# Kernel optimization log

Hardware: AMD Instinct MI355X
Metric: run time of the kernel (lower is better)

## Reference

```python
import jax, jax.numpy as jnp
import numpy as np

# BigBird-roberta-base config with block_size=64, 12 layers
B = 1; S = 2048; D = 768; F = 3072; V = 50358
L = 12; H = 12; HD = 64; BS = 64; NB = S // BS; R = 3
NEG = -1.0e9
NKB = 5 + R           # global(2) + window(3) + random(3) key blocks per query block
NK = NKB * BS         # gathered keys per query block


def _block_map(nb, r, seed=0):
    """Static per-query-block key-block indices + dedup mask (first occurrence kept)."""
    rng = np.random.default_rng(seed)
    idx = np.zeros((nb, 5 + r), np.int32)
    dedup = np.ones((nb, 5 + r), np.float32)
    for i in range(nb):
        lst = [0, nb - 1, max(i - 1, 0), i, min(i + 1, nb - 1)]
        cand = np.setdiff1d(np.arange(nb), np.array(lst))
        lst += list(rng.choice(cand, r, replace=False))
        seen = set()
        for j, b in enumerate(lst):
            idx[i, j] = int(b)
            if b in seen:
                dedup[i, j] = 0.0
            seen.add(int(b))
    return idx, dedup

BLK_IDX, BLK_DEDUP = _block_map(NB, R)


def layer_norm(x, s, b):
    m = jnp.mean(x, axis=-1, keepdims=True)
    v = jnp.mean(jnp.square(x - m), axis=-1, keepdims=True)
    return (x - m) * jax.lax.rsqrt(v + 1e-12) * s + b


def bigbird_attn(x, wq, wk, wv, bq, bk, bv, wo, bo, key_mask):
    # x: [B,S,D]; key_mask: [B,S] float (1=keep)
    q = (x @ wq + bq).reshape(B, S, H, HD).transpose(0, 2, 1, 3)  # [B,H,S,HD]
    k = (x @ wk + bk).reshape(B, S, H, HD).transpose(0, 2, 1, 3)
    v = (x @ wv + bv).reshape(B, S, H, HD).transpose(0, 2, 1, 3)
    scale = 1.0 / np.sqrt(HD)
    qb = q.reshape(B, H, NB, BS, HD)
    kb = k.reshape(B, H, NB, BS, HD)
    vb = v.reshape(B, H, NB, BS, HD)
    # gather sparse key/value blocks: [B,H,NB,NKB,BS,HD] -> [B,H,NB,NK,HD]
    kg = kb[:, :, BLK_IDX].reshape(B, H, NB, NK, HD)
    vg = vb[:, :, BLK_IDX].reshape(B, H, NB, NK, HD)
    scores = jnp.einsum('bhnqd,bhnkd->bhnqk', qb, kg) * scale  # [B,H,NB,BS,NK]
    kmb = key_mask.reshape(B, NB, BS)[:, BLK_IDX]               # [B,NB,NKB,BS]
    m = (kmb * BLK_DEDUP[None, :, :, None]).reshape(B, 1, NB, 1, NK)
    probs = jax.nn.softmax(scores + (1.0 - m) * NEG, axis=-1)
    ctx = jnp.einsum('bhnqk,bhnkd->bhnqd', probs, vg)           # [B,H,NB,BS,HD]
    # global query blocks (first & last) attend densely to all keys
    qg = jnp.concatenate([qb[:, :, 0], qb[:, :, -1]], axis=2)   # [B,H,2*BS,HD]
    sg = jnp.einsum('bhqd,bhkd->bhqk', qg, k) * scale
    sg = sg + (1.0 - key_mask[:, None, None, :]) * NEG
    cg = jnp.einsum('bhqk,bhkd->bhqd', jax.nn.softmax(sg, axis=-1), v)
    ctx = ctx.at[:, :, 0].set(cg[:, :, :BS]).at[:, :, -1].set(cg[:, :, BS:])
    ctx = ctx.reshape(B, H, S, HD).transpose(0, 2, 1, 3).reshape(B, S, D)
    return ctx @ wo + bo


def setup_inputs() -> dict:
    key = jax.random.key(0)
    ks = jax.random.split(key, 16)
    p = lambda k, shape: jax.random.normal(k, shape, jnp.float32) * 0.02
    return {
        'input_ids': jax.random.randint(ks[0], (B, S), 0, V),
        'attention_mask': jnp.ones((B, S), jnp.int32),
        'token_type_ids': jnp.zeros((B, S), jnp.int32),
        'word_emb': p(ks[1], (V, D)),
        'pos_emb': p(ks[2], (S, D)),
        'type_emb': p(ks[3], (2, D)),
        'emb_ln_s': jnp.ones((D,)), 'emb_ln_b': jnp.zeros((D,)),
        'Wq': p(ks[4], (L, D, D)), 'Wk': p(ks[5], (L, D, D)), 'Wv': p(ks[6], (L, D, D)),
        'bq': jnp.zeros((L, D)), 'bk': jnp.zeros((L, D)), 'bv': jnp.zeros((L, D)),
        'Wo': p(ks[7], (L, D, D)), 'bo': jnp.zeros((L, D)),
        'ln1_s': jnp.ones((L, D)), 'ln1_b': jnp.zeros((L, D)),
        'W1': p(ks[8], (L, D, F)), 'b1': jnp.zeros((L, F)),
        'W2': p(ks[9], (L, F, D)), 'b2': jnp.zeros((L, D)),
        'ln2_s': jnp.ones((L, D)), 'ln2_b': jnp.zeros((L, D)),
        'fc_w': p(ks[10], (D, V)), 'fc_b': jnp.zeros((V,)),
    }


def reference(input_ids, attention_mask, token_type_ids, word_emb, pos_emb, type_emb,
              emb_ln_s, emb_ln_b, Wq, Wk, Wv, bq, bk, bv, Wo, bo, ln1_s, ln1_b,
              W1, b1, W2, b2, ln2_s, ln2_b, fc_w, fc_b):
    x = word_emb[input_ids] + pos_emb[None] + type_emb[token_type_ids]
    x = layer_norm(x, emb_ln_s, emb_ln_b)
    km = attention_mask.astype(x.dtype)
    for l in range(L):
        a = bigbird_attn(x, Wq[l], Wk[l], Wv[l], bq[l], bk[l], bv[l], Wo[l], bo[l], km)
        x = layer_norm(x + a, ln1_s[l], ln1_b[l])
        hdd = jax.nn.gelu(x @ W1[l] + b1[l])
        x = layer_norm(x + hdd @ W2[l] + b2[l], ln2_s[l], ln2_b[l])
    return x @ fc_w + fc_b  # logits [B,S,V]
```

## Files before the change

### kernel.cpp

```cpp
#include <hip/hip_runtime.h>
#include <hip/hip_bf16.h>


#define S_LEN 2048
#define DMODEL 768
#define FFDIM 3072
#define VOCAB 50358
#define VPAD  50432
#define NLAYER 12
#define NHEAD 12
#define NB 32
#define NKB 8
#define QKVN 2304

typedef __attribute__((ext_vector_type(8))) short bfrag8;
typedef __attribute__((ext_vector_type(8))) unsigned short us8;
typedef __attribute__((ext_vector_type(4))) float facc4;

__device__ __forceinline__ unsigned short f2bf(float f) {
  unsigned int u = __builtin_bit_cast(unsigned int, f);
  u += 0x7fffu + ((u >> 16) & 1u);
  return (unsigned short)(u >> 16);
}
__device__ __forceinline__ float bf2f(unsigned short h) {
  unsigned int u = ((unsigned int)h) << 16;
  return __builtin_bit_cast(float, u);
}

#define MFMA16(a, b, c) __builtin_amdgcn_mfma_f32_16x16x32_bf16((a), (b), (c), 0, 0, 0)
#define GLDS16(g, l) __builtin_amdgcn_global_load_lds( \
    (const __attribute__((address_space(1))) void*)(g), \
    (__attribute__((address_space(3))) void*)(l), 16, 0, 0)

struct Pcg {
  unsigned long long hi, lo, inc_hi, inc_lo;
  int has32; unsigned int buf32;
};

__device__ __forceinline__ void pcg_step(Pcg& p) {
  const unsigned long long MH = 0x2360ed051fc65da4ull;
  const unsigned long long ML = 0x4385df649fccf645ull;
  unsigned long long rl = p.lo * ML;
  unsigned long long rh = __umul64hi(p.lo, ML) + p.lo * MH + p.hi * ML;
  unsigned long long nl = rl + p.inc_lo;
  unsigned long long nh = rh + p.inc_hi + (nl < rl ? 1ull : 0ull);
  p.lo = nl; p.hi = nh;
}
__device__ __forceinline__ unsigned long long pcg_next64(Pcg& p) {
  pcg_step(p);
  unsigned int rot = (unsigned int)(p.hi >> 58);
  unsigned long long x = p.hi ^ p.lo;
  return (x >> rot) | (x << ((64u - rot) & 63u));
}
__device__ __forceinline__ unsigned int pcg_next32(Pcg& p) {
  if (p.has32) { p.has32 = 0; return p.buf32; }
  unsigned long long n = pcg_next64(p);
  p.has32 = 1; p.buf32 = (unsigned int)(n >> 32);
  return (unsigned int)n;
}
__device__ __forceinline__ unsigned int lemire32(Pcg& p, unsigned int rng) {
  unsigned int rng_excl = rng + 1u;
  unsigned long long m = (unsigned long long)pcg_next32(p) * (unsigned long long)rng_excl;
  unsigned int leftover = (unsigned int)m;
  if (leftover < rng_excl) {
    unsigned int threshold = (0xffffffffu - rng) % rng_excl;
    while (leftover < threshold) {
      m = (unsigned long long)pcg_next32(p) * (unsigned long long)rng_excl;
      leftover = (unsigned int)m;
    }
  }
  return (unsigned int)(m >> 32);
}

__global__ void blockmap_kernel(int* __restrict__ blk_idx, float* __restrict__ dedup) {
  if (threadIdx.x != 0 || blockIdx.x != 0) return;
  unsigned int pool[4];
  unsigned int hc = 0x43b0d7e5u;
  auto ss_hash = [&hc](unsigned int val) {
    val ^= hc; hc *= 0x931e8875u; val *= hc; val ^= val >> 16; return val;
  };
  auto ss_mix = [](unsigned int x, unsigned int y) {
    unsigned int r = 0xca01f9ddu * x - 0x4973f715u * y;
    r ^= r >> 16; return r;
  };
  for (int i = 0; i < 4; ++i) pool[i] = ss_hash(0u);
  for (int s = 0; s < 4; ++s)
    for (int d = 0; d < 4; ++d)
      if (s != d) pool[d] = ss_mix(pool[d], ss_hash(pool[s]));
  unsigned int st32[8];
  unsigned int hb = 0x8b51f9ddu;
  for (int i = 0; i < 8; ++i) {
    unsigned int dv = pool[i & 3];
    dv ^= hb; hb *= 0x58f38dedu; dv *= hb; dv ^= dv >> 16;
    st32[i] = dv;
  }
  unsigned long long sd[4];
  for (int i = 0; i < 4; ++i)
    sd[i] = (unsigned long long)st32[2*i] | ((unsigned long long)st32[2*i+1] << 32);
  Pcg p;
  p.inc_hi = (sd[2] << 1) | (sd[3] >> 63);
  p.inc_lo = (sd[3] << 1) | 1ull;
  p.hi = 0ull; p.lo = 0ull;
  pcg_step(p);
  unsigned long long ol = p.lo;
  p.lo = ol + sd[1];
  p.hi = p.hi + sd[0] + (p.lo < ol ? 1ull : 0ull);
  pcg_step(p);
  p.has32 = 0; p.buf32 = 0;

  for (int i = 0; i < NB; ++i) {
    int lst[8];
    lst[0] = 0; lst[1] = NB - 1;
    lst[2] = (i > 0) ? i - 1 : 0;
    lst[3] = i;
    lst[4] = (i + 1 < NB - 1) ? i + 1 : NB - 1;
    bool excl[NB];
    for (int c = 0; c < NB; ++c) excl[c] = false;
    for (int j = 0; j < 5; ++j) excl[lst[j]] = true;
    int cand[NB], n = 0;
    for (int c = 0; c < NB; ++c) if (!excl[c]) cand[n++] = c;
    long long idx[3];
    unsigned long long hs[4] = {~0ull, ~0ull, ~0ull, ~0ull};
    for (int tI = 0; tI < 3; ++tI) {
      unsigned long long j = (unsigned long long)(n - 3 + tI);
      unsigned long long val = (unsigned long long)lemire32(p, (unsigned int)j);
      unsigned long long loc = val & 3ull;
      while (hs[loc] != ~0ull && hs[loc] != val) loc = (loc + 1ull) & 3ull;
      if (hs[loc] == ~0ull) { hs[loc] = val; idx[tI] = (long long)val; }
      else {
        loc = j & 3ull;
        while (hs[loc] != ~0ull) loc = (loc + 1ull) & 3ull;
        hs[loc] = j; idx[tI] = (long long)j;
      }
    }
    for (int fi = 2; fi >= 1; --fi) {
      int fj = (int)lemire32(p, (unsigned int)fi);
      long long tmpv = idx[fi]; idx[fi] = idx[fj]; idx[fj] = tmpv;
    }
    lst[5] = cand[idx[0]]; lst[6] = cand[idx[1]]; lst[7] = cand[idx[2]];

    unsigned int seen = 0u;
    for (int j = 0; j < 8; ++j) {
      blk_idx[i*8 + j] = lst[j];
      dedup[i*8 + j] = ((seen >> lst[j]) & 1u) ? 0.0f : 1.0f;
      seen |= (1u << lst[j]);
    }
  }
}

__global__ __launch_bounds__(256) void tconv_kernel(
    const float* __restrict__ src, unsigned short* __restrict__ dst,
    int K, int N, size_t src_stride, size_t dst_stride) {
  __shared__ float tile[64][65];
  src += (size_t)blockIdx.z * src_stride;
  dst += (size_t)blockIdx.z * dst_stride;
  int n0 = blockIdx.x * 64, k0 = blockIdx.y * 64;
  int t = threadIdx.x;
  int tr = t >> 4, tc = (t & 15) * 4;
  if ((N & 3) == 0 && n0 + 64 <= N) {
    #pragma unroll
    for (int i = 0; i < 4; ++i) {
      int k = k0 + tr + i * 16;
      float4 v = *reinterpret_cast<const float4*>(src + (size_t)k * N + n0 + tc);
      tile[tr + i*16][tc + 0] = v.x; tile[tr + i*16][tc + 1] = v.y;
      tile[tr + i*16][tc + 2] = v.z; tile[tr + i*16][tc + 3] = v.w;
    }
  } else if ((N & 1) == 0 && n0 + 64 <= N) {
    #pragma unroll
    for (int i = 0; i < 4; ++i) {
      int k = k0 + tr + i * 16;
      float2 v0 = *reinterpret_cast<const float2*>(src + (size_t)k * N + n0 + tc);
      float2 v1 = *reinterpret_cast<const float2*>(src + (size_t)k * N + n0 + tc + 2);
      tile[tr + i*16][tc + 0] = v0.x; tile[tr + i*16][tc + 1] = v0.y;
      tile[tr + i*16][tc + 2] = v1.x; tile[tr + i*16][tc + 3] = v1.y;
    }
  } else {
    for (int i = 0; i < 4; ++i) {
      int k = k0 + tr + i * 16;
      #pragma unroll
      for (int q2 = 0; q2 < 4; ++q2) {
        int n = n0 + tc + q2;
        tile[tr + i*16][tc + q2] = (n < N) ? src[(size_t)k * N + n] : 0.0f;
      }
    }
  }
  __syncthreads();
  int wr_ = t >> 2, wc_ = (t & 3) * 16;
  us8 w0, w1;
  #pragma unroll
  for (int j = 0; j < 8; ++j) {
    w0[j] = f2bf(tile[wc_ + j][wr_]);
    w1[j] = f2bf(tile[wc_ + 8 + j][wr_]);
  }
  size_t b = (size_t)(n0 + wr_) * K + k0 + wc_;
  *reinterpret_cast<us8*>(dst + b) = w0;
  *reinterpret_cast<us8*>(dst + b + 8) = w1;
}

__global__ void bias_cat_kernel(const float* __restrict__ bq, const float* __restrict__ bk,
                                const float* __restrict__ bv, float* __restrict__ dst) {
  int l = blockIdx.x;
  for (int i = threadIdx.x; i < QKVN; i += blockDim.x) {
    float v = (i < 768) ? bq[l*768 + i] : (i < 1536) ? bk[l*768 + i - 768] : bv[l*768 + i - 1536];
    dst[l*QKVN + i] = v;
  }
}

__device__ __forceinline__ float block_sum256(float v, float* red) {
  for (int off = 32; off > 0; off >>= 1) v += __shfl_down(v, off);
  int wv = threadIdx.x >> 6;
  if ((threadIdx.x & 63) == 0) red[wv] = v;
  __syncthreads();
  float r = red[0] + red[1] + red[2] + red[3];
  __syncthreads();
  return r;
}

__global__ void embed_ln_kernel(const int* __restrict__ ids, const int* __restrict__ tts,
                                const float* __restrict__ we, const float* __restrict__ pe,
                                const float* __restrict__ te, const float* __restrict__ lns,
                                const float* __restrict__ lnb, float* __restrict__ x,
                                unsigned short* __restrict__ xh) {
  __shared__ float red[4];
  int row = blockIdx.x, t = threadIdx.x;
  int id = ids[row], ty = tts[row];
  float e[3]; float s = 0.0f;
  for (int j = 0; j < 3; ++j) {
    int d = t + 256*j;
    e[j] = we[(size_t)id*DMODEL + d] + pe[(size_t)row*DMODEL + d] + te[(size_t)ty*DMODEL + d];
    s += e[j];
  }
  float mean = block_sum256(s, red) * (1.0f/768.0f);
  float vs = 0.0f;
  for (int j = 0; j < 3; ++j) { float dd = e[j] - mean; vs += dd*dd; }
  float var = block_sum256(vs, red) * (1.0f/768.0f);
  float inv = rsqrtf(var + 1e-12f);
  for (int j = 0; j < 3; ++j) {
    int d = t + 256*j;
    float val = (e[j] - mean) * inv * lns[d] + lnb[d];
    size_t idx = (size_t)row*DMODEL + d;
    x[idx] = val;
    xh[idx] = f2bf(val);
  }
}

__global__ void resln_kernel(float* __restrict__ x, const float* __restrict__ a,
                             const float* __restrict__ lns, const float* __restrict__ lnb,
                             unsigned short* __restrict__ xh) {
  __shared__ float red[4];
  int row = blockIdx.x, t = threadIdx.x;
  float e[3]; float s = 0.0f;
  for (int j = 0; j < 3; ++j) {
    int d = t + 256*j;
    e[j] = x[(size_t)row*DMODEL + d] + a[(size_t)row*DMODEL + d];
    s += e[j];
  }
  float mean = block_sum256(s, red) * (1.0f/768.0f);
  float vs = 0.0f;
  for (int j = 0; j < 3; ++j) { float dd = e[j] - mean; vs += dd*dd; }
  float var = block_sum256(vs, red) * (1.0f/768.0f);
  float inv = rsqrtf(var + 1e-12f);
  for (int j = 0; j < 3; ++j) {
    int d = t + 256*j;
    float val = (e[j] - mean) * inv * lns[d] + lnb[d];
    size_t idx = (size_t)row*DMODEL + d;
    x[idx] = val;
    xh[idx] = f2bf(val);
  }
}

template<int BM, int NBUF, int TN, int OMODE, int ACT>
__global__ __launch_bounds__(256) void gemm13_kernel(
    const unsigned short* __restrict__ A_g, const unsigned short* __restrict__ Bt,
    const float* __restrict__ bias,
    float* __restrict__ Cf, unsigned short* __restrict__ Ch,
    int K, int Nreal) {
  __shared__ alignas(16) unsigned short As[NBUF][BM][32];
  __shared__ alignas(16) unsigned short Bs[NBUF][TN][32];
  constexpr int MFR = BM / 32;
  constexpr int NFR = (TN == 128) ? 4 : 2;
  constexpr int ACALLS = BM / 64;
  constexpr int NLOADS = ACALLS + ((TN == 128) ? 2 : 1);
  constexpr int DEPTH = NBUF - 2;
  int t = threadIdx.x;
  int mb = (int)gridDim.x;
  int nwg = mb * (int)gridDim.y;
  int lin = (int)blockIdx.x + mb * (int)blockIdx.y;
  int cpx = nwg >> 3;
  int nl = (lin & 7) * cpx + (lin >> 3);
  int m0 = (nl % mb) * BM, n0 = (nl / mb) * TN;

  int wave = t >> 6, lane = t & 63, l16 = lane & 15, lk = lane >> 4;
  int wr = wave >> 1, wc = wave & 1;
  int row16 = lane >> 2, seg4 = lane & 3;
  const int srcoff = (seg4 ^ ((row16 >> 1) & 3)) * 8;
  const int swzrd = (lk ^ ((l16 >> 1) & 3)) * 8;

  const unsigned short* ag = A_g + (size_t)(m0 + wave*(BM/4) + row16) * K + srcoff;
  const unsigned short* bg = Bt + (size_t)(n0 + (TN == 128 ? wave*32 : wave*16) + row16) * K + srcoff;
  const size_t K16 = (size_t)16 * K;

  auto STAGE = [&](int buf, int kit) {
    int k0 = kit << 5;
    #pragma unroll
    for (int j = 0; j < ACALLS; ++j)
      GLDS16(ag + (size_t)j * K16 + k0, &As[buf][wave*(BM/4) + 16*j][0]);
    if constexpr (TN == 128) {
      GLDS16(bg + k0, &Bs[buf][wave*32][0]);
      GLDS16(bg + K16 + k0, &Bs[buf][wave*32 + 16][0]);
    } else {
      GLDS16(bg + k0, &Bs[buf][wave*16][0]);
    }
  };

  facc4 acc[MFR][NFR];
  #pragma unroll
  for (int mi = 0; mi < MFR; ++mi)
    #pragma unroll
    for (int ni = 0; ni < NFR; ++ni)
      acc[mi][ni] = (facc4){0.f, 0.f, 0.f, 0.f};

  const int nk = K >> 5;
  STAGE(0, 0);
  if constexpr (DEPTH == 2) STAGE(1, 1);
  int cur = 0;
  for (int it = 0; it < nk; ++it) {
    if constexpr (DEPTH == 2) {
      if (it + 2 < nk) {
        STAGE((cur + 2) % NBUF, it + 2);
        asm volatile("s_waitcnt vmcnt(%0)" :: "n"(2 * NLOADS) : "memory");
      } else if (it + 1 < nk) {
        asm volatile("s_waitcnt vmcnt(%0)" :: "n"(NLOADS) : "memory");
      } else {
        asm volatile("s_waitcnt vmcnt(0)" ::: "memory");
      }
    } else {
      if (it + 1 < nk) {
        STAGE((cur + 1) % NBUF, it + 1);
        asm volatile("s_waitcnt vmcnt(%0)" :: "n"(NLOADS) : "memory");
      } else {
        asm volatile("s_waitcnt vmcnt(0)" ::: "memory");
      }
    }
    __builtin_amdgcn_sched_barrier(0);
    __builtin_amdgcn_s_barrier();
    __builtin_amdgcn_sched_barrier(0);
    bfrag8 af[MFR], bf[NFR];
    #pragma unroll
    for (int mi = 0; mi < MFR; ++mi)
      af[mi] = *reinterpret_cast<const bfrag8*>(&As[cur][wr*(BM/2) + mi*16 + l16][swzrd]);
    #pragma unroll
    for (int ni = 0; ni < NFR; ++ni)
      bf[ni] = *reinterpret_cast<const bfrag8*>(&Bs[cur][(TN == 128 ? wc*64 : wc*32) + ni*16 + l16][swzrd]);
    #pragma unroll
    for (int mi = 0; mi < MFR; ++mi)
      #pragma unroll
      for (int ni = 0; ni < NFR; ++ni)
        acc[mi][ni] = MFMA16(af[mi], bf[ni], acc[mi][ni]);
    cur = (cur + 1) % NBUF;
  }

  #pragma unroll
  for (int mi = 0; mi < MFR; ++mi)
    #pragma unroll
    for (int ni = 0; ni < NFR; ++ni) {
      int col = n0 + (TN == 128 ? wc*64 : wc*32) + ni*16 + l16;
      if (col >= Nreal) continue;
      float bv = bias[col];
      #pragma unroll
      for (int r2 = 0; r2 < 4; ++r2) {
        int row = m0 + wr*(BM/2) + mi*16 + lk*4 + r2;
        float val = acc[mi][ni][r2] + bv;
        if (ACT == 1) {
          float xx = val;
          val = 0.5f * xx * (1.0f + tanhf(0.7978845608028654f * (xx + 0.044715f * xx * xx * xx)));
        }
        size_t idx = (size_t)row * Nreal + col;
        if (OMODE == 0) Cf[idx] = val;
        else Ch[idx] = f2bf(val);
      }
    }
}

__device__ __forceinline__ void stage_glds64_swz(unsigned short (*dst)[64],
    const unsigned short* __restrict__ src, int ld, int t) {
  int w = t >> 6, lane = t & 63;
  int row8 = lane >> 3;
  int seg = (lane & 7) ^ (row8 & 7);
  const unsigned short* s = src + (size_t)(w*16 + row8) * ld + seg * 8;
  GLDS16(s, &dst[w*16][0]);
  GLDS16(s + (size_t)8 * ld, &dst[w*16 + 8][0]);
}

__global__ __launch_bounds__(256) void attn_kernel(
    const unsigned short* __restrict__ qkvh,
    const int* __restrict__ blk_idx, const float* __restrict__ dedup,
    const int* __restrict__ amask,
    unsigned short* __restrict__ ctxh,
    float* __restrict__ go, float* __restrict__ gm, float* __restrict__ gl) {
  __shared__ alignas(16) unsigned short Qs[64][64];
  __shared__ alignas(16) unsigned short KV2[2][64][64];
  __shared__ alignas(16) unsigned short Vs[64][66];
  __shared__ alignas(16) unsigned short Pt[64][68];
  int h = blockIdx.y;
  int bx = (int)blockIdx.x;
  const bool is_glob = (bx >= 30);
  int g = is_glob ? ((bx - 30) >> 2) : 0;
  int part = is_glob ? ((bx - 30) & 3) : 0;
  int qi = is_glob ? (g ? (NB - 1) : 0) : (bx + 1);
  int t = threadIdx.x, wave = t >> 6, lane = t & 63, l16 = lane & 15, lk = lane >> 4;
  const int swq0 = ((lk ^ (l16 & 7))) * 8;
  const int swq1 = (((4 + lk) ^ (l16 & 7))) * 8;
  const int vrow = t >> 2, vcolb = (t & 3) * 16;

  int barr[8];
  float addm[8][4];
  #pragma unroll
  for (int kb = 0; kb < 8; ++kb)
    barr[kb] = is_glob ? (part*8 + kb) : blk_idx[qi*NKB + kb];
  #pragma unroll
  for (int kb = 0; kb < 8; ++kb) {
    float dd = is_glob ? 1.0f : dedup[qi*NKB + kb];
    #pragma unroll
    for (int ni = 0; ni < 4; ++ni) {
      float mk = (float)amask[barr[kb]*64 + ni*16 + l16] * dd;
      addm[kb][ni] = (1.0f - mk) * (-1.0e9f);
    }
  }

  stage_glds64_swz(Qs, qkvh + (size_t)(qi*64)*QKVN + h*64, QKVN, t);
  __syncthreads();
  const bfrag8 q0 = *reinterpret_cast<const bfrag8*>(&Qs[wave*16 + l16][swq0]);
  const bfrag8 q1 = *reinterpret_cast<const bfrag8*>(&Qs[wave*16 + l16][swq1]);

  float mrow[4] = {-3.0e38f, -3.0e38f, -3.0e38f, -3.0e38f};
  float lrow[4] = {0.f, 0.f, 0.f, 0.f};
  facc4 o[4];
  #pragma unroll
  for (int ni = 0; ni < 4; ++ni) o[ni] = (facc4){0.f, 0.f, 0.f, 0.f};

  stage_glds64_swz(KV2[0], qkvh + (size_t)(barr[0]*64)*QKVN + DMODEL + h*64, QKVN, t);
  __builtin_amdgcn_sched_barrier(0);
  us8 vA0, vA1, vB0, vB1;
  {
    const unsigned short* vs0 = qkvh + (size_t)(barr[0]*64 + vrow)*QKVN + 2*DMODEL + h*64 + vcolb;
    vA0 = *reinterpret_cast<const us8*>(vs0);
    vA1 = *reinterpret_cast<const us8*>(vs0 + 8);
  }

  auto body = [&](int kb, const us8& vc0, const us8& vc1, us8& vn0, us8& vn1) {
    if (kb + 1 < 8) {
      int bn = barr[kb + 1];
      stage_glds64_swz(KV2[(kb + 1) & 1], qkvh + (size_t)(bn*64)*QKVN + DMODEL + h*64, QKVN, t);
      __builtin_amdgcn_sched_barrier(0);
      const unsigned short* vsn = qkvh + (size_t)(bn*64 + vrow)*QKVN + 2*DMODEL + h*64 + vcolb;
      vn0 = *reinterpret_cast<const us8*>(vsn);
      vn1 = *reinterpret_cast<const us8*>(vsn + 8);
      asm volatile("s_waitcnt vmcnt(4)" ::: "memory");
    } else {
      asm volatile("s_waitcnt vmcnt(0)" ::: "memory");
    }
    __builtin_amdgcn_sched_barrier(0);
    __builtin_amdgcn_s_barrier();
    __builtin_amdgcn_sched_barrier(0);
    float s[4][4];
    #pragma unroll
    for (int ni = 0; ni < 4; ++ni) {
      bfrag8 k0 = *reinterpret_cast<const bfrag8*>(&KV2[kb & 1][ni*16 + l16][swq0]);
      bfrag8 k1 = *reinterpret_cast<const bfrag8*>(&KV2[kb & 1][ni*16 + l16][swq1]);
      facc4 sa = (facc4){0.f, 0.f, 0.f, 0.f};
      sa = MFMA16(q0, k0, sa);
      sa = MFMA16(q1, k1, sa);
      #pragma unroll
      for (int r = 0; r < 4; ++r) s[ni][r] = sa[r] * 0.125f + addm[kb][ni];
    }
    float pexp[4][4];
    #pragma unroll
    for (int r = 0; r < 4; ++r) {
      float tm = fmaxf(fmaxf(s[0][r], s[1][r]), fmaxf(s[2][r], s[3][r]));
      tm = fmaxf(tm, __shfl_xor(tm, 1));
      tm = fmaxf(tm, __shfl_xor(tm, 2));
      tm = fmaxf(tm, __shfl_xor(tm, 4));
      tm = fmaxf(tm, __shfl_xor(tm, 8));
      float mn = fmaxf(mrow[r], tm);
      float f = expf(mrow[r] - mn);
      #pragma unroll
      for (int ni = 0; ni < 4; ++ni) o[ni][r] *= f;
      float ps = 0.0f;
      #pragma unroll
      for (int ni = 0; ni < 4; ++ni) { pexp[ni][r] = expf(s[ni][r] - mn); ps += pexp[ni][r]; }
      ps += __shfl_xor(ps, 1);
      ps += __shfl_xor(ps, 2);
      ps += __shfl_xor(ps, 4);
      ps += __shfl_xor(ps, 8);
      lrow[r] = lrow[r] * f + ps;
      mrow[r] = mn;
    }
    #pragma unroll
    for (int ni = 0; ni < 4; ++ni)
      #pragma unroll
      for (int r = 0; r < 4; ++r)
        Pt[wave*16 + lk*4 + r][ni*16 + l16] = f2bf(pexp[ni][r]);
    #pragma unroll
    for (int j = 0; j < 8; ++j) {
      Vs[vcolb + j][vrow] = vc0[j];
      Vs[vcolb + 8 + j][vrow] = vc1[j];
    }
    asm volatile("s_waitcnt lgkmcnt(0)" ::: "memory");
    __builtin_amdgcn_sched_barrier(0);
    __builtin_amdgcn_s_barrier();
    __builtin_amdgcn_sched_barrier(0);
    #pragma unroll
    for (int kc = 0; kc < 2; ++kc) {
      bfrag8 ph = *reinterpret_cast<const bfrag8*>(&Pt[wave*16 + l16][kc*32 + lk*8]);
      #pragma unroll
      for (int ni = 0; ni < 4; ++ni) {
        bfrag8 vh = *reinterpret_cast<const bfrag8*>(&Vs[ni*16 + l16][kc*32 + lk*8]);
        o[ni] = MFMA16(ph, vh, o[ni]);
      }
    }
  };

  body(0, vA0, vA1, vB0, vB1);
  body(1, vB0, vB1, vA0, vA1);
  body(2, vA0, vA1, vB0, vB1);
  body(3, vB0, vB1, vA0, vA1);
  body(4, vA0, vA1, vB0, vB1);
  body(5, vB0, vB1, vA0, vA1);
  body(6, vA0, vA1, vB0, vB1);
  body(7, vB0, vB1, vA0, vA1);

  if (!is_glob) {
    float invl[4];
    #pragma unroll
    for (int r = 0; r < 4; ++r) invl[r] = 1.0f / lrow[r];
    #pragma unroll
    for (int ni = 0; ni < 4; ++ni)
      #pragma unroll
      for (int r = 0; r < 4; ++r) {
        int row = qi*64 + wave*16 + lk*4 + r;
        int col = h*64 + ni*16 + l16;
        ctxh[(size_t)row*DMODEL + col] = f2bf(o[ni][r] * invl[r]);
      }
  } else {
    int pidx = (g * NHEAD + h) * 4 + part;
    float* gob = go + (size_t)pidx * 64 * 64;
    #pragma unroll
    for (int ni = 0; ni < 4; ++ni)
      #pragma unroll
      for (int r = 0; r < 4; ++r)
        gob[(wave*16 + lk*4 + r) * 64 + ni*16 + l16] = o[ni][r];
    if (l16 == 0) {
      #pragma unroll
      for (int r = 0; r < 4; ++r) {
        int row = wave*16 + lk*4 + r;
        gm[pidx*64 + row] = mrow[r];
        gl[pidx*64 + row] = lrow[r];
      }
    }
  }
}

__global__ __launch_bounds__(256) void gattn_comb_kernel(
    const float* __restrict__ go, const float* __restrict__ gm,
    const float* __restrict__ gl, unsigned short* __restrict__ ctxh) {
  int g = blockIdx.x, h = blockIdx.y;
  int t = threadIdx.x;
  int row = t >> 2, cseg = (t & 3) * 16;
  int base = (g * NHEAD + h) * 4;
  float m = -3.0e38f;
  for (int p = 0; p < 4; ++p) m = fmaxf(m, gm[(base + p)*64 + row]);
  float w[4]; float l = 0.0f;
  for (int p = 0; p < 4; ++p) {
    w[p] = expf(gm[(base + p)*64 + row] - m);
    l += gl[(base + p)*64 + row] * w[p];
  }
  float inv = 1.0f / l;
  int qrow = (g ? (NB - 1) * 64 : 0) + row;
  for (int c = 0; c < 16; ++c) {
    float acc = 0.0f;
    for (int p = 0; p < 4; ++p)
      acc += go[((size_t)(base + p)*64 + row)*64 + cseg + c] * w[p];
    ctxh[(size_t)qrow*DMODEL + h*64 + cseg + c] = f2bf(acc * inv);
  }
}

extern "C" void kernel_launch(void* const* d_in, const int* in_sizes, int n_in,
                              void* d_out, int out_size, void* d_ws, size_t ws_size,
                              hipStream_t stream) {
  const int*   input_ids  = (const int*)d_in[0];
  const int*   attn_mask  = (const int*)d_in[1];
  const int*   token_type = (const int*)d_in[2];
  const float* word_emb   = (const float*)d_in[3];
  const float* pos_emb    = (const float*)d_in[4];
  const float* type_emb   = (const float*)d_in[5];
  const float* emb_ln_s   = (const float*)d_in[6];
  const float* emb_ln_b   = (const float*)d_in[7];
  const float* Wq = (const float*)d_in[8];
  const float* Wk = (const float*)d_in[9];
  const float* Wv = (const float*)d_in[10];
  const float* bq = (const float*)d_in[11];
  const float* bk = (const float*)d_in[12];
  const float* bv = (const float*)d_in[13];
  const float* Wo = (const float*)d_in[14];
  const float* bo = (const float*)d_in[15];
  const float* ln1_s = (const float*)d_in[16];
  const float* ln1_b = (const float*)d_in[17];
  const float* W1 = (const float*)d_in[18];
  const float* b1 = (const float*)d_in[19];
  const float* W2 = (const float*)d_in[20];
  const float* b2 = (const float*)d_in[21];
  const float* ln2_s = (const float*)d_in[22];
  const float* ln2_b = (const float*)d_in[23];
  const float* fc_w = (const float*)d_in[24];
  const float* fc_b = (const float*)d_in[25];
  float* out = (float*)d_out;

  unsigned char* base = (unsigned char*)d_ws;
  size_t off = 0;
  auto carve = [&](size_t bytes) -> void* {
    void* p = base + off;
    off = (off + bytes + 255) & ~(size_t)255;
    return p;
  };
  int*   blk_i = (int*)carve(256 * 4);
  float* dedup = (float*)carve(256 * 4);
  float* bqkv  = (float*)carve((size_t)NLAYER * QKVN * 4);
  float* x     = (float*)carve((size_t)S_LEN * DMODEL * 4);
  float* tmp   = (float*)carve((size_t)S_LEN * DMODEL * 4);
  unsigned short* xh   = (unsigned short*)carve((size_t)S_LEN * DMODEL * 2);
  unsigned short* qkvh = (unsigned short*)carve((size_t)S_LEN * QKVN * 2);
  unsigned short* ctxh = (unsigned short*)carve((size_t)S_LEN * DMODEL * 2);
  unsigned short* hbh  = (unsigned short*)carve((size_t)S_LEN * FFDIM * 2);
  float* go    = (float*)carve((size_t)2 * NHEAD * 4 * 64 * 64 * 4);
  float* gm    = (float*)carve((size_t)2 * NHEAD * 4 * 64 * 4);
  float* gl    = (float*)carve((size_t)2 * NHEAD * 4 * 64 * 4);
  unsigned short* qkvT = (unsigned short*)carve((size_t)NLAYER * QKVN * DMODEL * 2);
  unsigned short* woT  = (unsigned short*)carve((size_t)NLAYER * DMODEL * DMODEL * 2);
  unsigned short* w1T  = (unsigned short*)carve((size_t)NLAYER * FFDIM * DMODEL * 2);
  unsigned short* w2T  = (unsigned short*)carve((size_t)NLAYER * DMODEL * FFDIM * 2);
  unsigned short* fcT  = (unsigned short*)carve((size_t)VPAD * DMODEL * 2);

  blockmap_kernel<<<1, 1, 0, stream>>>(blk_i, dedup);

  const size_t DD = (size_t)DMODEL * DMODEL;
  dim3 g768(12, 12, NLAYER);
  tconv_kernel<<<g768, 256, 0, stream>>>(Wq, qkvT + 0,            DMODEL, DMODEL, DD, (size_t)QKVN * DMODEL);
  tconv_kernel<<<g768, 256, 0, stream>>>(Wk, qkvT + 768 * DMODEL, DMODEL, DMODEL, DD, (size_t)QKVN * DMODEL);
  tconv_kernel<<<g768, 256, 0, stream>>>(Wv, qkvT + 1536 * DMODEL,DMODEL, DMODEL, DD, (size_t)QKVN * DMODEL);
  tconv_kernel<<<g768, 256, 0, stream>>>(Wo, woT, DMODEL, DMODEL, DD, DD);
  tconv_kernel<<<dim3(48, 12, NLAYER), 256, 0, stream>>>(W1, w1T, DMODEL, FFDIM, (size_t)DMODEL * FFDIM, (size_t)FFDIM * DMODEL);
  tconv_kernel<<<dim3(12, 48, NLAYER), 256, 0, stream>>>(W2, w2T, FFDIM, DMODEL, (size_t)FFDIM * DMODEL, (size_t)DMODEL * FFDIM);
  tconv_kernel<<<dim3(VPAD / 64, 12, 1), 256, 0, stream>>>(fc_w, fcT, DMODEL, VOCAB, 0, 0);
  bias_cat_kernel<<<NLAYER, 256, 0, stream>>>(bq, bk, bv, bqkv);

  embed_ln_kernel<<<S_LEN, 256, 0, stream>>>(input_ids, token_type, word_emb, pos_emb,
                                             type_emb, emb_ln_s, emb_ln_b, x, xh);

  for (int l = 0; l < NLAYER; ++l) {
    gemm13_kernel<64, 4, 128, 2, 0><<<dim3(32, QKVN/128), 256, 0, stream>>>(
        xh, qkvT + (size_t)l * QKVN * DMODEL, bqkv + (size_t)l * QKVN,
        nullptr, qkvh, DMODEL, QKVN);

    attn_kernel<<<dim3(38, NHEAD), 256, 0, stream>>>(
        qkvh, blk_i, dedup, attn_mask, ctxh, go, gm, gl);
    gattn_comb_kernel<<<dim3(2, NHEAD), 256, 0, stream>>>(go, gm, gl, ctxh);

    gemm13_kernel<64, 4, 64, 0, 0><<<dim3(32, DMODEL/64), 256, 0, stream>>>(
        ctxh, woT + (size_t)l * DD, bo + (size_t)l * DMODEL,
        tmp, nullptr, DMODEL, DMODEL);
    resln_kernel<<<S_LEN, 256, 0, stream>>>(x, tmp, ln1_s + l*DMODEL, ln1_b + l*DMODEL, xh);

    gemm13_kernel<64, 4, 128, 2, 1><<<dim3(32, FFDIM/128), 256, 0, stream>>>(
        xh, w1T + (size_t)l * FFDIM * DMODEL, b1 + (size_t)l * FFDIM,
        nullptr, hbh, DMODEL, FFDIM);
    gemm13_kernel<64, 4, 64, 0, 0><<<dim3(32, DMODEL/64), 256, 0, stream>>>(
        hbh, w2T + (size_t)l * DMODEL * FFDIM, b2 + (size_t)l * DMODEL,
        tmp, nullptr, FFDIM, DMODEL);
    resln_kernel<<<S_LEN, 256, 0, stream>>>(x, tmp, ln2_s + l*DMODEL, ln2_b + l*DMODEL, xh);
  }

  gemm13_kernel<128, 3, 128, 0, 0><<<dim3(16, VPAD/128), 256, 0, stream>>>(
      xh, fcT, fc_b, out, nullptr, DMODEL, VOCAB);
}
```

Before: 2.367 ms.

## Widen GEMM N-tile to 256 and fuse residual add into GEMM epilogue

Generalizes the GEMM kernel to arbitrary N-tile widths and uses 256-wide tiles for the QKV and FFN1 projections, increasing A-tile reuse per workgroup. It also adds the residual input in the output GEMM epilogue so the layernorm kernel reads only one tensor. Larger tiles raise LDS and register use and reduce the workgroup count, which may hurt occupancy and load balance.

```diff
diff --git a/kernel.cpp b/kernel.cpp
--- a/kernel.cpp
+++ b/kernel.cpp
@@ -252,7 +252,7 @@
   float e[3]; float s = 0.0f;
   for (int j = 0; j < 3; ++j) {
     int d = t + 256*j;
-    e[j] = x[(size_t)row*DMODEL + d] + a[(size_t)row*DMODEL + d];
+    e[j] = a[(size_t)row*DMODEL + d];
     s += e[j];
   }
   float mean = block_sum256(s, red) * (1.0f/768.0f);
@@ -269,18 +269,19 @@
   }
 }
 
-template<int BM, int NBUF, int TN, int OMODE, int ACT>
-__global__ __launch_bounds__(256) void gemm13_kernel(
+template<int BM, int NBUF, int TN, int OMODE, int ACT, int RES>
+__global__ __launch_bounds__(256) void gemm14_kernel(
     const unsigned short* __restrict__ A_g, const unsigned short* __restrict__ Bt,
-    const float* __restrict__ bias,
+    const float* __restrict__ bias, const float* __restrict__ Rf,
     float* __restrict__ Cf, unsigned short* __restrict__ Ch,
     int K, int Nreal) {
   __shared__ alignas(16) unsigned short As[NBUF][BM][32];
   __shared__ alignas(16) unsigned short Bs[NBUF][TN][32];
   constexpr int MFR = BM / 32;
-  constexpr int NFR = (TN == 128) ? 4 : 2;
+  constexpr int NFR = TN / 32;
   constexpr int ACALLS = BM / 64;
-  constexpr int NLOADS = ACALLS + ((TN == 128) ? 2 : 1);
+  constexpr int BCALLS = TN / 64;
+  constexpr int NLOADS = ACALLS + BCALLS;
   constexpr int DEPTH = NBUF - 2;
   int t = threadIdx.x;
   int mb = (int)gridDim.x;
@@ -297,7 +298,7 @@
   const int swzrd = (lk ^ ((l16 >> 1) & 3)) * 8;
 
   const unsigned short* ag = A_g + (size_t)(m0 + wave*(BM/4) + row16) * K + srcoff;
-  const unsigned short* bg = Bt + (size_t)(n0 + (TN == 128 ? wave*32 : wave*16) + row16) * K + srcoff;
+  const unsigned short* bg = Bt + (size_t)(n0 + wave*(TN/4) + row16) * K + srcoff;
   const size_t K16 = (size_t)16 * K;
 
   auto STAGE = [&](int buf, int kit) {
@@ -305,12 +306,9 @@
     #pragma unroll
     for (int j = 0; j < ACALLS; ++j)
       GLDS16(ag + (size_t)j * K16 + k0, &As[buf][wave*(BM/4) + 16*j][0]);
-    if constexpr (TN == 128) {
-      GLDS16(bg + k0, &Bs[buf][wave*32][0]);
-      GLDS16(bg + K16 + k0, &Bs[buf][wave*32 + 16][0]);
-    } else {
-      GLDS16(bg + k0, &Bs[buf][wave*16][0]);
-    }
+    #pragma unroll
+    for (int j = 0; j < BCALLS; ++j)
+      GLDS16(bg + (size_t)j * K16 + k0, &Bs[buf][wave*(TN/4) + 16*j][0]);
   };
 
   facc4 acc[MFR][NFR];
@@ -351,7 +349,7 @@
       af[mi] = *reinterpret_cast<const bfrag8*>(&As[cur][wr*(BM/2) + mi*16 + l16][swzrd]);
     #pragma unroll
     for (int ni = 0; ni < NFR; ++ni)
-      bf[ni] = *reinterpret_cast<const bfrag8*>(&Bs[cur][(TN == 128 ? wc*64 : wc*32) + ni*16 + l16][swzrd]);
+      bf[ni] = *reinterpret_cast<const bfrag8*>(&Bs[cur][wc*(TN/2) + ni*16 + l16][swzrd]);
     #pragma unroll
     for (int mi = 0; mi < MFR; ++mi)
       #pragma unroll
@@ -364,7 +362,7 @@
   for (int mi = 0; mi < MFR; ++mi)
     #pragma unroll
     for (int ni = 0; ni < NFR; ++ni) {
-      int col = n0 + (TN == 128 ? wc*64 : wc*32) + ni*16 + l16;
+      int col = n0 + wc*(TN/2) + ni*16 + l16;
       if (col >= Nreal) continue;
       float bv = bias[col];
       #pragma unroll
@@ -376,8 +374,12 @@
           val = 0.5f * xx * (1.0f + tanhf(0.7978845608028654f * (xx + 0.044715f * xx * xx * xx)));
         }
         size_t idx = (size_t)row * Nreal + col;
-        if (OMODE == 0) Cf[idx] = val;
-        else Ch[idx] = f2bf(val);
+        if (OMODE == 0) {
+          if constexpr (RES) val += Rf[idx];
+          Cf[idx] = val;
+        } else {
+          Ch[idx] = f2bf(val);
+        }
       }
     }
 }
@@ -658,28 +660,28 @@
                                              type_emb, emb_ln_s, emb_ln_b, x, xh);
 
   for (int l = 0; l < NLAYER; ++l) {
-    gemm13_kernel<64, 4, 128, 2, 0><<<dim3(32, QKVN/128), 256, 0, stream>>>(
-        xh, qkvT + (size_t)l * QKVN * DMODEL, bqkv + (size_t)l * QKVN,
+    gemm14_kernel<64, 4, 256, 2, 0, 0><<<dim3(32, QKVN/256), 256, 0, stream>>>(
+        xh, qkvT + (size_t)l * QKVN * DMODEL, bqkv + (size_t)l * QKVN, nullptr,
         nullptr, qkvh, DMODEL, QKVN);
 
     attn_kernel<<<dim3(38, NHEAD), 256, 0, stream>>>(
         qkvh, blk_i, dedup, attn_mask, ctxh, go, gm, gl);
     gattn_comb_kernel<<<dim3(2, NHEAD), 256, 0, stream>>>(go, gm, gl, ctxh);
 
-    gemm13_kernel<64, 4, 64, 0, 0><<<dim3(32, DMODEL/64), 256, 0, stream>>>(
-        ctxh, woT + (size_t)l * DD, bo + (size_t)l * DMODEL,
+    gemm14_kernel<64, 4, 64, 0, 0, 1><<<dim3(32, DMODEL/64), 256, 0, stream>>>(
+        ctxh, woT + (size_t)l * DD, bo + (size_t)l * DMODEL, x,
         tmp, nullptr, DMODEL, DMODEL);
     resln_kernel<<<S_LEN, 256, 0, stream>>>(x, tmp, ln1_s + l*DMODEL, ln1_b + l*DMODEL, xh);
 
-    gemm13_kernel<64, 4, 128, 2, 1><<<dim3(32, FFDIM/128), 256, 0, stream>>>(
-        xh, w1T + (size_t)l * FFDIM * DMODEL, b1 + (size_t)l * FFDIM,
+    gemm14_kernel<64, 4, 256, 2, 1, 0><<<dim3(32, FFDIM/256), 256, 0, stream>>>(
+        xh, w1T + (size_t)l * FFDIM * DMODEL, b1 + (size_t)l * FFDIM, nullptr,
         nullptr, hbh, DMODEL, FFDIM);
-    gemm13_kernel<64, 4, 64, 0, 0><<<dim3(32, DMODEL/64), 256, 0, stream>>>(
-        hbh, w2T + (size_t)l * DMODEL * FFDIM, b2 + (size_t)l * DMODEL,
+    gemm14_kernel<64, 4, 64, 0, 0, 1><<<dim3(32, DMODEL/64), 256, 0, stream>>>(
+        hbh, w2T + (size_t)l * DMODEL * FFDIM, b2 + (size_t)l * DMODEL, x,
         tmp, nullptr, FFDIM, DMODEL);
     resln_kernel<<<S_LEN, 256, 0, stream>>>(x, tmp, ln2_s + l*DMODEL, ln2_b + l*DMODEL, xh);
   }
 
-  gemm13_kernel<128, 3, 128, 0, 0><<<dim3(16, VPAD/128), 256, 0, stream>>>(
-      xh, fcT, fc_b, out, nullptr, DMODEL, VOCAB);
-}
+  gemm14_kernel<128, 3, 128, 0, 0, 0><<<dim3(16, VPAD/128), 256, 0, stream>>>(
+      xh, fcT, fc_b, nullptr, out, nullptr, DMODEL, VOCAB);
+}
```

Result: slower. 2.485 ms (+5.0%).
